# Kernel optimization log

Measured on AMD Instinct MI355X. Metric: run time of the kernel, lower is better.

Reference implementation:

```python
import jax, jax.numpy as jnp
import numpy as np

N = 50000      # nodes
E = 800000     # edges (avg degree 16)
IN = 256       # in_features
HD = 4         # num_heads
D = 64         # out_features per head


def setup_inputs() -> dict:
    key = jax.random.key(0)
    k1, k2, k3, k4, k5 = jax.random.split(key, 5)
    h = jax.random.normal(k1, (N, IN), dtype=jnp.float32)
    edge_index = jax.random.randint(k2, (2, E), 0, N)
    # W stored as [in_features, num_heads*out_features] (h @ W == Linear(h))
    W = jax.random.normal(k3, (IN, HD * D), dtype=jnp.float32) * (1.0 / np.sqrt(IN))
    a_src = jax.random.normal(k4, (HD, D), dtype=jnp.float32) * 0.1
    a_dst = jax.random.normal(k5, (HD, D), dtype=jnp.float32) * 0.1
    return {"h": h, "edge_index": edge_index, "W": W, "a_src": a_src, "a_dst": a_dst}


def reference(h, edge_index, W, a_src, a_dst):
    n = h.shape[0]
    src, dst = edge_index[0], edge_index[1]
    # project: [N, H, D]
    hp = (h @ W).reshape(n, HD, D)
    # per-edge attention logits [E, H]
    e_src = jnp.einsum('ehd,hd->eh', hp[src], a_src)
    e_dst = jnp.einsum('ehd,hd->eh', hp[dst], a_dst)
    e = jax.nn.leaky_relu(e_src + e_dst, negative_slope=0.2)
    # segment softmax over incoming edges of each dst node
    e_max = jax.ops.segment_max(e, dst, num_segments=n)          # [N, H]
    ex = jnp.exp(e - e_max[dst])                                  # [E, H]
    e_sum = jax.ops.segment_sum(ex, dst, num_segments=n)         # [N, H]
    alpha = ex / (e_sum[dst] + 1e-16)                             # [E, H]
    # weighted aggregation
    msg = hp[src] * alpha[..., None]                              # [E, H, D]
    out = jax.ops.segment_sum(msg, dst, num_segments=n)          # [N, H, D]
    return out.reshape(n, HD * D)                                 # concat=True
```

## Files before the change

### kernel.cpp

```cpp
#include <hip/hip_runtime.h>

#define HD 4
#define D 64
#define NHD 256
#define N_IN 256

typedef __attribute__((ext_vector_type(8))) __bf16 bf16x8;
typedef __attribute__((ext_vector_type(4))) __bf16 bf16x4;
typedef __attribute__((ext_vector_type(4))) float f32x4;

constexpr int AROW = 40;

__global__ __launch_bounds__(256) void pre_kernel(const float* __restrict__ W,
                                                  __bf16* __restrict__ WtH,
                                                  __bf16* __restrict__ WtL,
                                                  const int* __restrict__ ei,
                                                  int* __restrict__ deg, int E) {
  const int b = blockIdx.x;
  if (b < N_IN) {
    const int k = b, n = threadIdx.x;
    float w = W[k * NHD + n];
    __bf16 hi = (__bf16)w;
    __bf16 lo = (__bf16)(w - (float)hi);
    WtH[n * N_IN + k] = hi;
    WtL[n * N_IN + k] = lo;
  } else {
    const int e = (b - N_IN) * 256 + threadIdx.x;
    if (e < E) atomicAdd(&deg[ei[E + e]], 1);
  }
}

__global__ __launch_bounds__(256) void gemm_scan_kernel(
    const float* __restrict__ A, const __bf16* __restrict__ WtH,
    const __bf16* __restrict__ WtL, const float* __restrict__ a_src,
    const float* __restrict__ a_dst, __bf16* __restrict__ hp16,
    float* __restrict__ s_out, float* __restrict__ t_out, int M,
    const int* __restrict__ deg, int* __restrict__ partial,
    int* __restrict__ blocksum, int NB, int MT) {
  __shared__ __bf16 As[128 * AROW];
  __shared__ __bf16 BsH[128 * AROW];
  __shared__ __bf16 BsL[128 * AROW];
  __shared__ int ws4[4];
  const int tid = threadIdx.x;

  if ((int)blockIdx.x < NB) {
    const int lane = tid & 63, wv = tid >> 6;
    const int base = blockIdx.x * 1024 + tid * 4;
    const int n = M;
    int v0 = (base + 0 < n) ? deg[base + 0] : 0;
    int v1 = (base + 1 < n) ? deg[base + 1] : 0;
    int v2 = (base + 2 < n) ? deg[base + 2] : 0;
    int v3 = (base + 3 < n) ? deg[base + 3] : 0;
    int sum = v0 + v1 + v2 + v3;
    int incl = sum;
#pragma unroll
    for (int off = 1; off < 64; off <<= 1) {
      int y = __shfl_up(incl, off);
      if (lane >= off) incl += y;
    }
    if (lane == 63) ws4[wv] = incl;
    __syncthreads();
    int wbase = 0;
#pragma unroll
    for (int w = 0; w < 4; ++w)
      if (w < wv) wbase += ws4[w];
    int excl = wbase + incl - sum;
    if (base + 0 < n) partial[base + 0] = excl;
    if (base + 1 < n) partial[base + 1] = excl + v0;
    if (base + 2 < n) partial[base + 2] = excl + v0 + v1;
    if (base + 3 < n) partial[base + 3] = excl + v0 + v1 + v2;
    if (tid == 255) blocksum[blockIdx.x] = wbase + incl;
    return;
  }

  const int g = blockIdx.x - NB;
  const int bx = g % MT, by = g / MT;
  const int lane = tid & 63, wv = tid >> 6;
  const int wr = wv >> 1, wc = wv & 1;
  const int c15 = lane & 15, quad = lane >> 4;
  const int m0 = bx * 128, n0 = by * 128;

  f32x4 acc[4][4];
#pragma unroll
  for (int i = 0; i < 4; ++i)
#pragma unroll
    for (int j = 0; j < 4; ++j) acc[i][j] = (f32x4){0.f, 0.f, 0.f, 0.f};

  const int am = tid >> 1, aks = (tid & 1) * 16;
  const int gr = m0 + am;
  const bool arow_ok = (gr < M);
  const float* Arow = &A[(size_t)gr * N_IN];
  const __bf16* BHrow = &WtH[(size_t)(n0 + am) * N_IN];
  const __bf16* BLrow = &WtL[(size_t)(n0 + am) * N_IN];

  for (int kc = 0; kc < 8; ++kc) {
    const int k0 = kc * 32;
    float4 f0, f1, f2, f3;
    if (arow_ok) {
      f0 = *(const float4*)&Arow[k0 + aks + 0];
      f1 = *(const float4*)&Arow[k0 + aks + 4];
      f2 = *(const float4*)&Arow[k0 + aks + 8];
      f3 = *(const float4*)&Arow[k0 + aks + 12];
    } else {
      f0 = f1 = f2 = f3 = make_float4(0.f, 0.f, 0.f, 0.f);
    }
    bf16x8 bh0 = *(const bf16x8*)&BHrow[k0 + aks];
    bf16x8 bh1 = *(const bf16x8*)&BHrow[k0 + aks + 8];
    bf16x8 bl0 = *(const bf16x8*)&BLrow[k0 + aks];
    bf16x8 bl1 = *(const bf16x8*)&BLrow[k0 + aks + 8];

    __syncthreads();
    bf16x8 a0, a1;
    a0[0] = (__bf16)f0.x; a0[1] = (__bf16)f0.y; a0[2] = (__bf16)f0.z; a0[3] = (__bf16)f0.w;
    a0[4] = (__bf16)f1.x; a0[5] = (__bf16)f1.y; a0[6] = (__bf16)f1.z; a0[7] = (__bf16)f1.w;
    a1[0] = (__bf16)f2.x; a1[1] = (__bf16)f2.y; a1[2] = (__bf16)f2.z; a1[3] = (__bf16)f2.w;
    a1[4] = (__bf16)f3.x; a1[5] = (__bf16)f3.y; a1[6] = (__bf16)f3.z; a1[7] = (__bf16)f3.w;
    *(bf16x8*)&As[am * AROW + aks + 0] = a0;
    *(bf16x8*)&As[am * AROW + aks + 8] = a1;
    *(bf16x8*)&BsH[am * AROW + aks + 0] = bh0;
    *(bf16x8*)&BsH[am * AROW + aks + 8] = bh1;
    *(bf16x8*)&BsL[am * AROW + aks + 0] = bl0;
    *(bf16x8*)&BsL[am * AROW + aks + 8] = bl1;
    __syncthreads();

    bf16x8 af[4], bfh[4], bfl[4];
#pragma unroll
    for (int i = 0; i < 4; ++i) {
      af[i]  = *(bf16x8*)&As[(wr * 64 + i * 16 + c15) * AROW + quad * 8];
      bfh[i] = *(bf16x8*)&BsH[(wc * 64 + i * 16 + c15) * AROW + quad * 8];
      bfl[i] = *(bf16x8*)&BsL[(wc * 64 + i * 16 + c15) * AROW + quad * 8];
    }
#pragma unroll
    for (int mi = 0; mi < 4; ++mi)
#pragma unroll
      for (int ni = 0; ni < 4; ++ni)
        acc[mi][ni] = __builtin_amdgcn_mfma_f32_16x16x32_bf16(af[mi], bfh[ni], acc[mi][ni], 0, 0, 0);
#pragma unroll
    for (int mi = 0; mi < 4; ++mi)
#pragma unroll
      for (int ni = 0; ni < 4; ++ni)
        acc[mi][ni] = __builtin_amdgcn_mfma_f32_16x16x32_bf16(af[mi], bfl[ni], acc[mi][ni], 0, 0, 0);
  }

  const int head = by * 2 + wc;
  float av[4], ad[4];
#pragma unroll
  for (int ni = 0; ni < 4; ++ni) {
    av[ni] = a_src[head * D + ni * 16 + c15];
    ad[ni] = a_dst[head * D + ni * 16 + c15];
  }
  const int row0w = m0 + wr * 64;
#pragma unroll
  for (int mi = 0; mi < 4; ++mi) {
#pragma unroll
    for (int j = 0; j < 4; ++j) {
      float ps = acc[mi][0][j] * av[0] + acc[mi][1][j] * av[1] +
                 acc[mi][2][j] * av[2] + acc[mi][3][j] * av[3];
      float pt = acc[mi][0][j] * ad[0] + acc[mi][1][j] * ad[1] +
                 acc[mi][2][j] * ad[2] + acc[mi][3][j] * ad[3];
#pragma unroll
      for (int m = 1; m < 16; m <<= 1) {
        ps += __shfl_xor(ps, m);
        pt += __shfl_xor(pt, m);
      }
      const int row = row0w + mi * 16 + quad * 4 + j;
      if (c15 == 0 && row < M) {
        s_out[row * HD + head] = ps;
        t_out[row * HD + head] = pt;
      }
    }
#pragma unroll
    for (int ni = 0; ni < 4; ++ni) {
#pragma unroll
      for (int j = 0; j < 4; ++j) {
        const int row = row0w + mi * 16 + quad * 4 + j;
        const int col = n0 + wc * 64 + ni * 16 + c15;
        if (row < M) hp16[(size_t)row * NHD + col] = (__bf16)acc[mi][ni][j];
      }
    }
  }
}

__global__ __launch_bounds__(256) void scan23_kernel(const int* __restrict__ partial,
                                                     const int* __restrict__ blocksum,
                                                     int* __restrict__ row_ptr,
                                                     int* __restrict__ cursor, int n, int NB) {
  __shared__ int s_off;
  const int tid = threadIdx.x;
  if (tid < 64) {
    int v = (tid < NB) ? blocksum[tid] : 0;
    int incl = v;
#pragma unroll
    for (int off = 1; off < 64; off <<= 1) {
      int y = __shfl_up(incl, off);
      if (tid >= off) incl += y;
    }
    int prev = __shfl_up(incl, 1);
    int excl = (tid == 0) ? 0 : prev;
    if (tid == (int)blockIdx.x) s_off = excl;
    if (blockIdx.x == 0 && tid == NB - 1) row_ptr[n] = incl;
  }
  __syncthreads();
  const int off = s_off;
  const int base = blockIdx.x * 1024 + tid * 4;
  if (base + 3 < n) {
    int4 p = *(const int4*)&partial[base];
    int4 r = make_int4(p.x + off, p.y + off, p.z + off, p.w + off);
    *(int4*)&row_ptr[base] = r;
    *(int4*)&cursor[base] = r;
  } else {
    for (int j = 0; j < 4; ++j)
      if (base + j < n) {
        int r = partial[base + j] + off;
        row_ptr[base + j] = r;
        cursor[base + j] = r;
      }
  }
}

__global__ void scatter_kernel(const int* __restrict__ ei, int* __restrict__ cursor,
                               int* __restrict__ csr_src, int E) {
  int e = blockIdx.x * blockDim.x + threadIdx.x;
  if (e >= E) return;
  int sn = ei[e], dn = ei[E + e];
  int pos = atomicAdd(&cursor[dn], 1);
  csr_src[pos] = sn;
}

__global__ __launch_bounds__(256) void aggregate_kernel(
    const int* __restrict__ row_ptr, const int* __restrict__ csr_src,
    const float* __restrict__ s, const float* __restrict__ t,
    const __bf16* __restrict__ hp16, float* __restrict__ out, int N) {
  const int wave = threadIdx.x >> 6;
  const int lane = threadIdx.x & 63;
  const int node = blockIdx.x * 4 + wave;
  if (node >= N) return;
  const int h = lane >> 4;
  const int d0 = lane * 4;
  const int beg = row_ptr[node], end = row_ptr[node + 1];
  const float tn = t[node * HD + h];
  float num0 = 0.f, num1 = 0.f, num2 = 0.f, num3 = 0.f, den = 0.f;
  int i = beg;
  for (; i + 8 <= end; i += 8) {
    int sn0 = csr_src[i], sn1 = csr_src[i + 1], sn2 = csr_src[i + 2], sn3 = csr_src[i + 3];
    int sn4 = csr_src[i + 4], sn5 = csr_src[i + 5], sn6 = csr_src[i + 6], sn7 = csr_src[i + 7];
    bf16x4 v0 = *(const bf16x4*)&hp16[(size_t)sn0 * NHD + d0];
    bf16x4 v1 = *(const bf16x4*)&hp16[(size_t)sn1 * NHD + d0];
    bf16x4 v2 = *(const bf16x4*)&hp16[(size_t)sn2 * NHD + d0];
    bf16x4 v3 = *(const bf16x4*)&hp16[(size_t)sn3 * NHD + d0];
    bf16x4 v4 = *(const bf16x4*)&hp16[(size_t)sn4 * NHD + d0];
    bf16x4 v5 = *(const bf16x4*)&hp16[(size_t)sn5 * NHD + d0];
    bf16x4 v6 = *(const bf16x4*)&hp16[(size_t)sn6 * NHD + d0];
    bf16x4 v7 = *(const bf16x4*)&hp16[(size_t)sn7 * NHD + d0];
    float lg0 = s[sn0 * HD + h] + tn, lg1 = s[sn1 * HD + h] + tn;
    float lg2 = s[sn2 * HD + h] + tn, lg3 = s[sn3 * HD + h] + tn;
    float lg4 = s[sn4 * HD + h] + tn, lg5 = s[sn5 * HD + h] + tn;
    float lg6 = s[sn6 * HD + h] + tn, lg7 = s[sn7 * HD + h] + tn;
    lg0 = fmaxf(lg0, 0.2f * lg0); lg1 = fmaxf(lg1, 0.2f * lg1);
    lg2 = fmaxf(lg2, 0.2f * lg2); lg3 = fmaxf(lg3, 0.2f * lg3);
    lg4 = fmaxf(lg4, 0.2f * lg4); lg5 = fmaxf(lg5, 0.2f * lg5);
    lg6 = fmaxf(lg6, 0.2f * lg6); lg7 = fmaxf(lg7, 0.2f * lg7);
    float ex0 = __expf(lg0), ex1 = __expf(lg1), ex2 = __expf(lg2), ex3 = __expf(lg3);
    float ex4 = __expf(lg4), ex5 = __expf(lg5), ex6 = __expf(lg6), ex7 = __expf(lg7);
    den += ((ex0 + ex1) + (ex2 + ex3)) + ((ex4 + ex5) + (ex6 + ex7));
    num0 += ex0 * (float)v0[0] + ex1 * (float)v1[0] + ex2 * (float)v2[0] + ex3 * (float)v3[0]
          + ex4 * (float)v4[0] + ex5 * (float)v5[0] + ex6 * (float)v6[0] + ex7 * (float)v7[0];
    num1 += ex0 * (float)v0[1] + ex1 * (float)v1[1] + ex2 * (float)v2[1] + ex3 * (float)v3[1]
          + ex4 * (float)v4[1] + ex5 * (float)v5[1] + ex6 * (float)v6[1] + ex7 * (float)v7[1];
    num2 += ex0 * (float)v0[2] + ex1 * (float)v1[2] + ex2 * (float)v2[2] + ex3 * (float)v3[2]
          + ex4 * (float)v4[2] + ex5 * (float)v5[2] + ex6 * (float)v6[2] + ex7 * (float)v7[2];
    num3 += ex0 * (float)v0[3] + ex1 * (float)v1[3] + ex2 * (float)v2[3] + ex3 * (float)v3[3]
          + ex4 * (float)v4[3] + ex5 * (float)v5[3] + ex6 * (float)v6[3] + ex7 * (float)v7[3];
  }
  for (; i < end; ++i) {
    int sn0 = csr_src[i];
    bf16x4 v0 = *(const bf16x4*)&hp16[(size_t)sn0 * NHD + d0];
    float lg0 = s[sn0 * HD + h] + tn;
    lg0 = fmaxf(lg0, 0.2f * lg0);
    float ex0 = __expf(lg0);
    den += ex0;
    num0 += ex0 * (float)v0[0];
    num1 += ex0 * (float)v0[1];
    num2 += ex0 * (float)v0[2];
    num3 += ex0 * (float)v0[3];
  }
  const float inv = 1.0f / (den + 1e-16f);
  float4 o = make_float4(num0 * inv, num1 * inv, num2 * inv, num3 * inv);
  *(float4*)&out[(size_t)node * NHD + d0] = o;
}

extern "C" void kernel_launch(void* const* d_in, const int* in_sizes, int n_in,
                              void* d_out, int out_size, void* d_ws, size_t ws_size,
                              hipStream_t stream) {
  const float* h_ptr  = (const float*)d_in[0];
  const int*   ei     = (const int*)d_in[1];
  const float* W      = (const float*)d_in[2];
  const float* a_src  = (const float*)d_in[3];
  const float* a_dst  = (const float*)d_in[4];
  float* out = (float*)d_out;

  const int N = in_sizes[0] / N_IN;
  const int E = in_sizes[1] / 2;
  const int NB = (N + 1023) / 1024;
  const int MT = (N + 127) / 128;

  auto align256 = [](size_t x) { return (x + 255) & ~size_t(255); };
  char* base = (char*)d_ws;
  size_t off = 0;
  __bf16* hp16 = (__bf16*)(base + off);  off += align256((size_t)N * NHD * 2);
  __bf16* WtH  = (__bf16*)(base + off);  off += align256((size_t)N_IN * NHD * 2);
  __bf16* WtL  = (__bf16*)(base + off);  off += align256((size_t)N_IN * NHD * 2);
  float* s       = (float*)(base + off); off += align256((size_t)N * HD * 4);
  float* t       = (float*)(base + off); off += align256((size_t)N * HD * 4);
  int*   deg     = (int*)(base + off);   off += align256((size_t)N * 4);
  int*   partial = (int*)(base + off);   off += align256((size_t)N * 4);
  int*   blocksum= (int*)(base + off);   off += align256((size_t)NB * 4);
  int*   row_ptr = (int*)(base + off);   off += align256((size_t)(N + 1) * 4);
  int*   cursor  = (int*)(base + off);   off += align256((size_t)N * 4);
  int*   csr_src = (int*)(base + off);   off += align256((size_t)E * 4);

  hipMemsetAsync(deg, 0, (size_t)N * 4, stream);
  pre_kernel<<<N_IN + (E + 255) / 256, 256, 0, stream>>>(W, WtH, WtL, ei, deg, E);
  gemm_scan_kernel<<<NB + MT * 2, 256, 0, stream>>>(h_ptr, WtH, WtL, a_src, a_dst,
                                                    hp16, s, t, N, deg, partial,
                                                    blocksum, NB, MT);
  scan23_kernel<<<NB, 256, 0, stream>>>(partial, blocksum, row_ptr, cursor, N, NB);
  scatter_kernel<<<(E + 255) / 256, 256, 0, stream>>>(ei, cursor, csr_src, E);
  aggregate_kernel<<<(N + 3) / 4, 256, 0, stream>>>(row_ptr, csr_src, s, t, hp16, out, N);
}
```

Before: 291.4 us.

## Drop split-bf16 weight correction, shard degree/cursor atomics, shrink aggregate unroll

The GEMM previously split W into high and low bf16 parts and ran two MFMA passes. Now it uses a single bf16 copy of W, halving the MFMA work and the B-tile shared-memory traffic at the cost of projection accuracy. Degree counting and CSR scatter atomics are spread over 8 replicated counter arrays keyed by block index, to reduce atomic contention on hot nodes. This adds memset and read traffic for the 8x arrays. The aggregation inner loop unroll drops from 8 to 4 edges.

Result: faster. 275.3 us (-5.5%).

```diff
diff --git a/kernel.cpp b/kernel.cpp
--- a/kernel.cpp
+++ b/kernel.cpp
@@ -12,46 +12,46 @@
 constexpr int AROW = 40;
 
 __global__ __launch_bounds__(256) void pre_kernel(const float* __restrict__ W,
-                                                  __bf16* __restrict__ WtH,
-                                                  __bf16* __restrict__ WtL,
+                                                  __bf16* __restrict__ Wt,
                                                   const int* __restrict__ ei,
-                                                  int* __restrict__ deg, int E) {
+                                                  int* __restrict__ deg8, int Nn, int E) {
   const int b = blockIdx.x;
   if (b < N_IN) {
     const int k = b, n = threadIdx.x;
-    float w = W[k * NHD + n];
-    __bf16 hi = (__bf16)w;
-    __bf16 lo = (__bf16)(w - (float)hi);
-    WtH[n * N_IN + k] = hi;
-    WtL[n * N_IN + k] = lo;
+    Wt[n * N_IN + k] = (__bf16)W[k * NHD + n];
   } else {
     const int e = (b - N_IN) * 256 + threadIdx.x;
-    if (e < E) atomicAdd(&deg[ei[E + e]], 1);
+    const int c = b & 7;
+    if (e < E) atomicAdd(&deg8[c * Nn + ei[E + e]], 1);
   }
 }
 
 __global__ __launch_bounds__(256) void gemm_scan_kernel(
-    const float* __restrict__ A, const __bf16* __restrict__ WtH,
-    const __bf16* __restrict__ WtL, const float* __restrict__ a_src,
-    const float* __restrict__ a_dst, __bf16* __restrict__ hp16,
-    float* __restrict__ s_out, float* __restrict__ t_out, int M,
-    const int* __restrict__ deg, int* __restrict__ partial,
+    const float* __restrict__ A, const __bf16* __restrict__ Wt,
+    const float* __restrict__ a_src, const float* __restrict__ a_dst,
+    __bf16* __restrict__ hp16, float* __restrict__ s_out, float* __restrict__ t_out,
+    int M, const int* __restrict__ deg8, int* __restrict__ partial,
     int* __restrict__ blocksum, int NB, int MT) {
   __shared__ __bf16 As[128 * AROW];
-  __shared__ __bf16 BsH[128 * AROW];
-  __shared__ __bf16 BsL[128 * AROW];
+  __shared__ __bf16 Bs[128 * AROW];
   __shared__ int ws4[4];
   const int tid = threadIdx.x;
 
   if ((int)blockIdx.x < NB) {
     const int lane = tid & 63, wv = tid >> 6;
     const int base = blockIdx.x * 1024 + tid * 4;
-    const int n = M;
-    int v0 = (base + 0 < n) ? deg[base + 0] : 0;
-    int v1 = (base + 1 < n) ? deg[base + 1] : 0;
-    int v2 = (base + 2 < n) ? deg[base + 2] : 0;
-    int v3 = (base + 3 < n) ? deg[base + 3] : 0;
-    int sum = v0 + v1 + v2 + v3;
+    int v[4];
+#pragma unroll
+    for (int j = 0; j < 4; ++j) {
+      int n = base + j;
+      int sum = 0;
+      if (n < M) {
+#pragma unroll
+        for (int c = 0; c < 8; ++c) sum += deg8[c * M + n];
+      }
+      v[j] = sum;
+    }
+    int sum = v[0] + v[1] + v[2] + v[3];
     int incl = sum;
 #pragma unroll
     for (int off = 1; off < 64; off <<= 1) {
@@ -65,10 +65,10 @@
     for (int w = 0; w < 4; ++w)
       if (w < wv) wbase += ws4[w];
     int excl = wbase + incl - sum;
-    if (base + 0 < n) partial[base + 0] = excl;
-    if (base + 1 < n) partial[base + 1] = excl + v0;
-    if (base + 2 < n) partial[base + 2] = excl + v0 + v1;
-    if (base + 3 < n) partial[base + 3] = excl + v0 + v1 + v2;
+    if (base + 0 < M) partial[base + 0] = excl;
+    if (base + 1 < M) partial[base + 1] = excl + v[0];
+    if (base + 2 < M) partial[base + 2] = excl + v[0] + v[1];
+    if (base + 3 < M) partial[base + 3] = excl + v[0] + v[1] + v[2];
     if (tid == 255) blocksum[blockIdx.x] = wbase + incl;
     return;
   }
@@ -90,8 +90,7 @@
   const int gr = m0 + am;
   const bool arow_ok = (gr < M);
   const float* Arow = &A[(size_t)gr * N_IN];
-  const __bf16* BHrow = &WtH[(size_t)(n0 + am) * N_IN];
-  const __bf16* BLrow = &WtL[(size_t)(n0 + am) * N_IN];
+  const __bf16* Brow = &Wt[(size_t)(n0 + am) * N_IN];
 
   for (int kc = 0; kc < 8; ++kc) {
     const int k0 = kc * 32;
@@ -104,10 +103,8 @@
     } else {
       f0 = f1 = f2 = f3 = make_float4(0.f, 0.f, 0.f, 0.f);
     }
-    bf16x8 bh0 = *(const bf16x8*)&BHrow[k0 + aks];
-    bf16x8 bh1 = *(const bf16x8*)&BHrow[k0 + aks + 8];
-    bf16x8 bl0 = *(const bf16x8*)&BLrow[k0 + aks];
-    bf16x8 bl1 = *(const bf16x8*)&BLrow[k0 + aks + 8];
+    bf16x8 b0 = *(const bf16x8*)&Brow[k0 + aks];
+    bf16x8 b1 = *(const bf16x8*)&Brow[k0 + aks + 8];
 
     __syncthreads();
     bf16x8 a0, a1;
@@ -117,29 +114,21 @@
     a1[4] = (__bf16)f3.x; a1[5] = (__bf16)f3.y; a1[6] = (__bf16)f3.z; a1[7] = (__bf16)f3.w;
     *(bf16x8*)&As[am * AROW + aks + 0] = a0;
     *(bf16x8*)&As[am * AROW + aks + 8] = a1;
-    *(bf16x8*)&BsH[am * AROW + aks + 0] = bh0;
-    *(bf16x8*)&BsH[am * AROW + aks + 8] = bh1;
-    *(bf16x8*)&BsL[am * AROW + aks + 0] = bl0;
-    *(bf16x8*)&BsL[am * AROW + aks + 8] = bl1;
+    *(bf16x8*)&Bs[am * AROW + aks + 0] = b0;
+    *(bf16x8*)&Bs[am * AROW + aks + 8] = b1;
     __syncthreads();
 
-    bf16x8 af[4], bfh[4], bfl[4];
+    bf16x8 af[4], bf_[4];
 #pragma unroll
     for (int i = 0; i < 4; ++i) {
       af[i]  = *(bf16x8*)&As[(wr * 64 + i * 16 + c15) * AROW + quad * 8];
-      bfh[i] = *(bf16x8*)&BsH[(wc * 64 + i * 16 + c15) * AROW + quad * 8];
-      bfl[i] = *(bf16x8*)&BsL[(wc * 64 + i * 16 + c15) * AROW + quad * 8];
+      bf_[i] = *(bf16x8*)&Bs[(wc * 64 + i * 16 + c15) * AROW + quad * 8];
     }
 #pragma unroll
     for (int mi = 0; mi < 4; ++mi)
 #pragma unroll
       for (int ni = 0; ni < 4; ++ni)
-        acc[mi][ni] = __builtin_amdgcn_mfma_f32_16x16x32_bf16(af[mi], bfh[ni], acc[mi][ni], 0, 0, 0);
-#pragma unroll
-    for (int mi = 0; mi < 4; ++mi)
-#pragma unroll
-      for (int ni = 0; ni < 4; ++ni)
-        acc[mi][ni] = __builtin_amdgcn_mfma_f32_16x16x32_bf16(af[mi], bfl[ni], acc[mi][ni], 0, 0, 0);
+        acc[mi][ni] = __builtin_amdgcn_mfma_f32_16x16x32_bf16(af[mi], bf_[ni], acc[mi][ni], 0, 0, 0);
   }
 
   const int head = by * 2 + wc;
@@ -183,8 +172,9 @@
 
 __global__ __launch_bounds__(256) void scan23_kernel(const int* __restrict__ partial,
                                                      const int* __restrict__ blocksum,
+                                                     const int* __restrict__ deg8,
                                                      int* __restrict__ row_ptr,
-                                                     int* __restrict__ cursor, int n, int NB) {
+                                                     int* __restrict__ cursor8, int n, int NB) {
   __shared__ int s_off;
   const int tid = threadIdx.x;
   if (tid < 64) {
@@ -203,27 +193,29 @@
   __syncthreads();
   const int off = s_off;
   const int base = blockIdx.x * 1024 + tid * 4;
-  if (base + 3 < n) {
-    int4 p = *(const int4*)&partial[base];
-    int4 r = make_int4(p.x + off, p.y + off, p.z + off, p.w + off);
-    *(int4*)&row_ptr[base] = r;
-    *(int4*)&cursor[base] = r;
-  } else {
-    for (int j = 0; j < 4; ++j)
-      if (base + j < n) {
-        int r = partial[base + j] + off;
-        row_ptr[base + j] = r;
-        cursor[base + j] = r;
-      }
-  }
-}
-
-__global__ void scatter_kernel(const int* __restrict__ ei, int* __restrict__ cursor,
-                               int* __restrict__ csr_src, int E) {
+#pragma unroll
+  for (int j = 0; j < 4; ++j) {
+    const int node = base + j;
+    if (node < n) {
+      int rp = partial[node] + off;
+      row_ptr[node] = rp;
+      int run = rp;
+#pragma unroll
+      for (int c = 0; c < 8; ++c) {
+        cursor8[c * n + node] = run;
+        run += deg8[c * n + node];
+      }
+    }
+  }
+}
+
+__global__ void scatter_kernel(const int* __restrict__ ei, int* __restrict__ cursor8,
+                               int* __restrict__ csr_src, int Nn, int E) {
   int e = blockIdx.x * blockDim.x + threadIdx.x;
   if (e >= E) return;
+  const int c = blockIdx.x & 7;
   int sn = ei[e], dn = ei[E + e];
-  int pos = atomicAdd(&cursor[dn], 1);
+  int pos = atomicAdd(&cursor8[c * Nn + dn], 1);
   csr_src[pos] = sn;
 }
 
@@ -241,36 +233,26 @@
   const float tn = t[node * HD + h];
   float num0 = 0.f, num1 = 0.f, num2 = 0.f, num3 = 0.f, den = 0.f;
   int i = beg;
-  for (; i + 8 <= end; i += 8) {
+  for (; i + 4 <= end; i += 4) {
     int sn0 = csr_src[i], sn1 = csr_src[i + 1], sn2 = csr_src[i + 2], sn3 = csr_src[i + 3];
-    int sn4 = csr_src[i + 4], sn5 = csr_src[i + 5], sn6 = csr_src[i + 6], sn7 = csr_src[i + 7];
     bf16x4 v0 = *(const bf16x4*)&hp16[(size_t)sn0 * NHD + d0];
     bf16x4 v1 = *(const bf16x4*)&hp16[(size_t)sn1 * NHD + d0];
     bf16x4 v2 = *(const bf16x4*)&hp16[(size_t)sn2 * NHD + d0];
     bf16x4 v3 = *(const bf16x4*)&hp16[(size_t)sn3 * NHD + d0];
-    bf16x4 v4 = *(const bf16x4*)&hp16[(size_t)sn4 * NHD + d0];
-    bf16x4 v5 = *(const bf16x4*)&hp16[(size_t)sn5 * NHD + d0];
-    bf16x4 v6 = *(const bf16x4*)&hp16[(size_t)sn6 * NHD + d0];
-    bf16x4 v7 = *(const bf16x4*)&hp16[(size_t)sn7 * NHD + d0];
-    float lg0 = s[sn0 * HD + h] + tn, lg1 = s[sn1 * HD + h] + tn;
-    float lg2 = s[sn2 * HD + h] + tn, lg3 = s[sn3 * HD + h] + tn;
-    float lg4 = s[sn4 * HD + h] + tn, lg5 = s[sn5 * HD + h] + tn;
-    float lg6 = s[sn6 * HD + h] + tn, lg7 = s[sn7 * HD + h] + tn;
-    lg0 = fmaxf(lg0, 0.2f * lg0); lg1 = fmaxf(lg1, 0.2f * lg1);
-    lg2 = fmaxf(lg2, 0.2f * lg2); lg3 = fmaxf(lg3, 0.2f * lg3);
-    lg4 = fmaxf(lg4, 0.2f * lg4); lg5 = fmaxf(lg5, 0.2f * lg5);
-    lg6 = fmaxf(lg6, 0.2f * lg6); lg7 = fmaxf(lg7, 0.2f * lg7);
+    float lg0 = s[sn0 * HD + h] + tn;
+    float lg1 = s[sn1 * HD + h] + tn;
+    float lg2 = s[sn2 * HD + h] + tn;
+    float lg3 = s[sn3 * HD + h] + tn;
+    lg0 = fmaxf(lg0, 0.2f * lg0);
+    lg1 = fmaxf(lg1, 0.2f * lg1);
+    lg2 = fmaxf(lg2, 0.2f * lg2);
+    lg3 = fmaxf(lg3, 0.2f * lg3);
     float ex0 = __expf(lg0), ex1 = __expf(lg1), ex2 = __expf(lg2), ex3 = __expf(lg3);
-    float ex4 = __expf(lg4), ex5 = __expf(lg5), ex6 = __expf(lg6), ex7 = __expf(lg7);
-    den += ((ex0 + ex1) + (ex2 + ex3)) + ((ex4 + ex5) + (ex6 + ex7));
-    num0 += ex0 * (float)v0[0] + ex1 * (float)v1[0] + ex2 * (float)v2[0] + ex3 * (float)v3[0]
-          + ex4 * (float)v4[0] + ex5 * (float)v5[0] + ex6 * (float)v6[0] + ex7 * (float)v7[0];
-    num1 += ex0 * (float)v0[1] + ex1 * (float)v1[1] + ex2 * (float)v2[1] + ex3 * (float)v3[1]
-          + ex4 * (float)v4[1] + ex5 * (float)v5[1] + ex6 * (float)v6[1] + ex7 * (float)v7[1];
-    num2 += ex0 * (float)v0[2] + ex1 * (float)v1[2] + ex2 * (float)v2[2] + ex3 * (float)v3[2]
-          + ex4 * (float)v4[2] + ex5 * (float)v5[2] + ex6 * (float)v6[2] + ex7 * (float)v7[2];
-    num3 += ex0 * (float)v0[3] + ex1 * (float)v1[3] + ex2 * (float)v2[3] + ex3 * (float)v3[3]
-          + ex4 * (float)v4[3] + ex5 * (float)v5[3] + ex6 * (float)v6[3] + ex7 * (float)v7[3];
+    den += (ex0 + ex1) + (ex2 + ex3);
+    num0 += ex0 * (float)v0[0] + ex1 * (float)v1[0] + ex2 * (float)v2[0] + ex3 * (float)v3[0];
+    num1 += ex0 * (float)v0[1] + ex1 * (float)v1[1] + ex2 * (float)v2[1] + ex3 * (float)v3[1];
+    num2 += ex0 * (float)v0[2] + ex1 * (float)v1[2] + ex2 * (float)v2[2] + ex3 * (float)v3[2];
+    num3 += ex0 * (float)v0[3] + ex1 * (float)v1[3] + ex2 * (float)v2[3] + ex3 * (float)v3[3];
   }
   for (; i < end; ++i) {
     int sn0 = csr_src[i];
@@ -308,23 +290,22 @@
   char* base = (char*)d_ws;
   size_t off = 0;
   __bf16* hp16 = (__bf16*)(base + off);  off += align256((size_t)N * NHD * 2);
-  __bf16* WtH  = (__bf16*)(base + off);  off += align256((size_t)N_IN * NHD * 2);
-  __bf16* WtL  = (__bf16*)(base + off);  off += align256((size_t)N_IN * NHD * 2);
+  __bf16* Wt   = (__bf16*)(base + off);  off += align256((size_t)N_IN * NHD * 2);
   float* s       = (float*)(base + off); off += align256((size_t)N * HD * 4);
   float* t       = (float*)(base + off); off += align256((size_t)N * HD * 4);
-  int*   deg     = (int*)(base + off);   off += align256((size_t)N * 4);
+  int*   deg8    = (int*)(base + off);   off += align256((size_t)N * 8 * 4);
+  int*   cursor8 = (int*)(base + off);   off += align256((size_t)N * 8 * 4);
   int*   partial = (int*)(base + off);   off += align256((size_t)N * 4);
   int*   blocksum= (int*)(base + off);   off += align256((size_t)NB * 4);
   int*   row_ptr = (int*)(base + off);   off += align256((size_t)(N + 1) * 4);
-  int*   cursor  = (int*)(base + off);   off += align256((size_t)N * 4);
   int*   csr_src = (int*)(base + off);   off += align256((size_t)E * 4);
 
-  hipMemsetAsync(deg, 0, (size_t)N * 4, stream);
-  pre_kernel<<<N_IN + (E + 255) / 256, 256, 0, stream>>>(W, WtH, WtL, ei, deg, E);
-  gemm_scan_kernel<<<NB + MT * 2, 256, 0, stream>>>(h_ptr, WtH, WtL, a_src, a_dst,
-                                                    hp16, s, t, N, deg, partial,
+  hipMemsetAsync(deg8, 0, (size_t)N * 8 * 4, stream);
+  pre_kernel<<<N_IN + (E + 255) / 256, 256, 0, stream>>>(W, Wt, ei, deg8, N, E);
+  gemm_scan_kernel<<<NB + MT * 2, 256, 0, stream>>>(h_ptr, Wt, a_src, a_dst,
+                                                    hp16, s, t, N, deg8, partial,
                                                     blocksum, NB, MT);
-  scan23_kernel<<<NB, 256, 0, stream>>>(partial, blocksum, row_ptr, cursor, N, NB);
-  scatter_kernel<<<(E + 255) / 256, 256, 0, stream>>>(ei, cursor, csr_src, E);
+  scan23_kernel<<<NB, 256, 0, stream>>>(partial, blocksum, deg8, row_ptr, cursor8, N, NB);
+  scatter_kernel<<<(E + 255) / 256, 256, 0, stream>>>(ei, cursor8, csr_src, N, E);
   aggregate_kernel<<<(N + 3) / 4, 256, 0, stream>>>(row_ptr, csr_src, s, t, hp16, out, N);
 }
```
